# Performance work log

Hardware: AMD Instinct MI355X
Metric: run time of the kernel (lower is better)

Reference implementation:

```python
import jax, jax.numpy as jnp
import numpy as np

NUM_TOKENS = 8192
EMBED_DIM = 32
BETA = 1.0
DECAY = 0.99
L2_EPS = 1e-12  # torch F.normalize denom clamp


def l2norm(t):
    return t / jnp.maximum(jnp.linalg.norm(t, axis=-1, keepdims=True), L2_EPS)


def setup_inputs() -> dict:
    key = jax.random.key(0)
    k1, k2 = jax.random.split(key)
    z = jax.random.normal(k1, (32, EMBED_DIM, 16, 16), dtype=jnp.float32)  # [B, C, H, W]
    embedding = l2norm(jax.random.normal(k2, (NUM_TOKENS, EMBED_DIM), dtype=jnp.float32))
    cluster_sizes = jnp.zeros((NUM_TOKENS,), dtype=jnp.float32)
    return {"z": z, "embedding": embedding, "cluster_sizes": cluster_sizes}


def reference(z, embedding, cluster_sizes):
    B, C, H, W = z.shape
    zc = jnp.transpose(z, (0, 2, 3, 1))          # channel_last: [B, H, W, C]
    zn = l2norm(zc)
    z_flat = zn.reshape(-1, C)                   # [N, C], N = B*H*W

    # nearest centroid by cosine similarity (codebook rows are unit norm)
    cos_sim = z_flat @ embedding.T               # [N, K]
    token_ids = jnp.argmax(cos_sim, axis=-1)     # [N]
    z_q_flat = embedding[token_ids]              # gather, [N, C]
    z_q = z_q_flat.reshape(zn.shape)

    # EMA statistics (training branch; one-hot @ matmuls expressed as scatter-adds)
    bins = jnp.zeros((NUM_TOKENS,), z.dtype).at[token_ids].add(1.0)      # encodings.sum(0)
    new_cluster_sizes = cluster_sizes * DECAY + (1.0 - DECAY) * bins
    zero_mask = bins == 0
    bins_c = jnp.where(zero_mask, 1.0, bins)
    embed_sum = jnp.zeros((NUM_TOKENS, C), z.dtype).at[token_ids].add(z_flat)  # (z_flat.T @ onehot).T
    embed_normalized = l2norm(embed_sum / bins_c[:, None])
    embed_normalized = jnp.where(zero_mask[:, None], embedding, embed_normalized)
    new_embedding = l2norm(embedding * DECAY + (1.0 - DECAY) * embed_normalized)

    # commitment loss + straight-through estimator
    loss = BETA * jnp.mean((jax.lax.stop_gradient(z_q) - zn) ** 2)
    z_q_st = zn + jax.lax.stop_gradient(z_q - zn)
    z_q_out = jnp.transpose(z_q_st, (0, 3, 1, 2))  # back to [B, C, H, W]

    return (z_q_out, loss, token_ids.reshape(B, H, W), new_embedding, new_cluster_sizes)
```

## Files before the change

### kernel.cpp

```cpp
#include <hip/hip_runtime.h>


#define NTOK   8192
#define NCODE  8192
#define CDIM   32
#define HW     256
#define DECAYF 0.99f
#define EPSF   0.01f

#define OUT_ZQ   0
#define OUT_LOSS 262144
#define OUT_IDS  262145
#define OUT_EMB  270337
#define OUT_CS   532481

#define WS_ZN     0u
#define WS_ZNBF   1048576u
#define WS_EBF    1572864u
#define WS_BINS   2097152u
#define WS_LOSSP  2129920u
#define WS_IDS    2130176u
#define WS_POS    2162944u
#define WS_OFFS   2195712u
#define WS_SORTED 2228480u

typedef __attribute__((ext_vector_type(8))) short bf16x8;
typedef __attribute__((ext_vector_type(4))) float f32x4;

__device__ inline unsigned short f2bf(float x) {
    unsigned u = __float_as_uint(x);
    return (unsigned short)((u + 0x7FFFu + ((u >> 16) & 1u)) >> 16);
}
__device__ inline unsigned fmap(float s) {
    unsigned u = __float_as_uint(s);
    return (u & 0x80000000u) ? ~u : (u | 0x80000000u);
}

__global__ __launch_bounds__(256) void k_prep(const float* __restrict__ z,
                                              const float* __restrict__ emb,
                                              float* __restrict__ zn,
                                              unsigned short* __restrict__ znbf,
                                              unsigned short* __restrict__ ebf,
                                              int* __restrict__ bins,
                                              float* __restrict__ loss_part) {
    int bid = blockIdx.x, t = threadIdx.x;
    if (bid < 32) {
        int n = bid * 256 + t;
        int b = n >> 8, hw = n & 255;
        const float* zp = z + (size_t)b * (CDIM * HW) + hw;
        float v[CDIM];
        float ss = 0.f;
#pragma unroll
        for (int c = 0; c < CDIM; ++c) {
            float tv = zp[c * HW];
            v[c] = tv;
            ss += tv * tv;
        }
        float d = fmaxf(sqrtf(ss), 1e-12f);
        float* o = zn + (size_t)n * CDIM;
        unsigned short* ob = znbf + (size_t)n * CDIM;
#pragma unroll
        for (int c = 0; c < CDIM; ++c) {
            float tv = v[c] / d;
            o[c] = tv;
            ob[c] = f2bf(tv);
        }
    } else if (bid < 160) {
        int base = (bid - 32) * 2048 + t * 8;
        const float4* s = (const float4*)(emb + base);
        float4 x4 = s[0], y4 = s[1];
        ushort4 u0 = {f2bf(x4.x), f2bf(x4.y), f2bf(x4.z), f2bf(x4.w)};
        ushort4 u1 = {f2bf(y4.x), f2bf(y4.y), f2bf(y4.z), f2bf(y4.w)};
        *(ushort4*)(ebf + base) = u0;
        *(ushort4*)(ebf + base + 4) = u1;
    } else if (bid < 164) {
        int base = (bid - 160) * 2048 + t;
#pragma unroll
        for (int j = 0; j < 8; ++j) bins[base + j * 256] = 0;
    } else {
        if (t < 64) loss_part[t] = 0.f;
    }
}

__global__ __launch_bounds__(256) void k_argmax(const unsigned short* __restrict__ znbf,
                                                const unsigned short* __restrict__ ebf,
                                                const float* __restrict__ zn,
                                                const float* __restrict__ emb,
                                                int* __restrict__ bins,
                                                int* __restrict__ ids,
                                                int* __restrict__ pos,
                                                float* __restrict__ out,
                                                float* __restrict__ loss_part) {
    __shared__ float gm[4][16];
    __shared__ float thr[16];
    __shared__ unsigned long long bk[16];
    __shared__ int sid[16];
    __shared__ float ls4[4];

    int blk = blockIdx.x, t = threadIdx.x;
    int wave = t >> 6, lane = t & 63;
    int col = lane & 15, quad = lane >> 4;
    int tok0 = blk * 16;

    bf16x8 a = *(const bf16x8*)(znbf + (size_t)(tok0 + col) * CDIM + quad * 8);

    const f32x4 zero4 = {0.f, 0.f, 0.f, 0.f};
    int wbase = wave * 2048;

    float m0 = -1e30f, m1 = -1e30f, m2 = -1e30f, m3 = -1e30f;
#pragma unroll 4
    for (int tt = 0; tt < 128; ++tt) {
        int code = wbase + tt * 16 + col;
        bf16x8 b = *(const bf16x8*)(ebf + (size_t)code * CDIM + quad * 8);
        f32x4 d = __builtin_amdgcn_mfma_f32_16x16x32_bf16(a, b, zero4, 0, 0, 0);
        m0 = fmaxf(m0, d[0]); m1 = fmaxf(m1, d[1]);
        m2 = fmaxf(m2, d[2]); m3 = fmaxf(m3, d[3]);
    }
    {
        float mm[4] = {m0, m1, m2, m3};
#pragma unroll
        for (int r = 0; r < 4; ++r) {
            float v = mm[r];
#pragma unroll
            for (int s = 1; s < 16; s <<= 1) v = fmaxf(v, __shfl_xor(v, s));
            if (col == 0) gm[wave][quad * 4 + r] = v;
        }
    }
    if (t < 16) bk[t] = 0ull;
    __syncthreads();
    if (t < 16)
        thr[t] = fmaxf(fmaxf(gm[0][t], gm[1][t]), fmaxf(gm[2][t], gm[3][t])) - EPSF;
    __syncthreads();

    float th0 = thr[quad * 4 + 0], th1 = thr[quad * 4 + 1];
    float th2 = thr[quad * 4 + 2], th3 = thr[quad * 4 + 3];

#pragma unroll 4
    for (int tt = 0; tt < 128; ++tt) {
        int code = wbase + tt * 16 + col;
        bf16x8 b = *(const bf16x8*)(ebf + (size_t)code * CDIM + quad * 8);
        f32x4 d = __builtin_amdgcn_mfma_f32_16x16x32_bf16(a, b, zero4, 0, 0, 0);
#pragma unroll
        for (int r = 0; r < 4; ++r) {
            float dv = d[r];
            float tv = (r == 0) ? th0 : (r == 1) ? th1 : (r == 2) ? th2 : th3;
            if (dv >= tv) {
                int tl = quad * 4 + r;
                const float* zp = zn + (size_t)(tok0 + tl) * CDIM;
                const float* ep = emb + (size_t)code * CDIM;
                float a0 = 0.f, a1 = 0.f, a2 = 0.f, a3 = 0.f;
#pragma unroll
                for (int j = 0; j < 8; ++j) {
                    a0 = __builtin_fmaf(zp[4 * j + 0], ep[4 * j + 0], a0);
                    a1 = __builtin_fmaf(zp[4 * j + 1], ep[4 * j + 1], a1);
                    a2 = __builtin_fmaf(zp[4 * j + 2], ep[4 * j + 2], a2);
                    a3 = __builtin_fmaf(zp[4 * j + 3], ep[4 * j + 3], a3);
                }
                float s = (a0 + a1) + (a2 + a3);
                unsigned long long key = ((unsigned long long)fmap(s) << 13) |
                                         (unsigned long long)(8191 - code);
                atomicMax(&bk[tl], key);
            }
        }
    }
    __syncthreads();

    if (t < 16) {
        int id = 8191 - (int)(bk[t] & 8191ull);
        sid[t] = id;
        int n = tok0 + t;
        ids[n] = id;
        out[OUT_IDS + n] = (float)id;
        pos[n] = atomicAdd(bins + id, 1);
    }
    __syncthreads();

    float s = 0.f;
#pragma unroll
    for (int i = 0; i < 2; ++i) {
        int tl = i * 8 + (t >> 5);
        int c = t & 31;
        int n = tok0 + tl;
        int id = sid[tl];
        float ev = emb[(size_t)id * CDIM + c];
        float zv = zn[(size_t)n * CDIM + c];
        int b = n >> 8, hw = n & 255;
        out[OUT_ZQ + ((size_t)b * CDIM + c) * HW + hw] = ev;
        float dd = ev - zv;
        s += dd * dd;
    }
#pragma unroll
    for (int off = 32; off > 0; off >>= 1) s += __shfl_down(s, off);
    if (lane == 0) ls4[wave] = s;
    __syncthreads();
    if (t == 0)
        atomicAdd(loss_part + (blk & 63), ls4[0] + ls4[1] + ls4[2] + ls4[3]);
}

__global__ __launch_bounds__(1024) void k_scanplace(const int* __restrict__ bins,
                                                    const int* __restrict__ ids,
                                                    const int* __restrict__ pos,
                                                    int* __restrict__ offs,
                                                    int* __restrict__ sorted) {
    __shared__ int wtot[16], wexcl[16];
    int t = threadIdx.x;
    int lane = t & 63, wid = t >> 6;
    int loc[8];
    int s = 0;
#pragma unroll
    for (int i = 0; i < 8; ++i) {
        loc[i] = s;
        s += bins[t * 8 + i];
    }
    int v = s;
#pragma unroll
    for (int sh = 1; sh < 64; sh <<= 1) {
        int o = __shfl_up(v, sh);
        if (lane >= sh) v += o;
    }
    if (lane == 63) wtot[wid] = v;
    __syncthreads();
    if (t < 16) {
        int w = wtot[t];
        int iv = w;
#pragma unroll
        for (int sh = 1; sh < 16; sh <<= 1) {
            int o = __shfl_up(iv, sh);
            if (t >= sh) iv += o;
        }
        wexcl[t] = iv - w;
    }
    __syncthreads();
    int excl = wexcl[wid] + (v - s);
#pragma unroll
    for (int i = 0; i < 8; ++i) offs[t * 8 + i] = excl + loc[i];
    __syncthreads();
    for (int n = t; n < NTOK; n += 1024)
        sorted[offs[ids[n]] + pos[n]] = n;
}

__global__ __launch_bounds__(256) void k_update(const float* __restrict__ zn,
                                                const float* __restrict__ emb,
                                                const float* __restrict__ cs,
                                                const int* __restrict__ bins,
                                                const int* __restrict__ offs,
                                                const int* __restrict__ sorted,
                                                const float* __restrict__ loss_part,
                                                float* __restrict__ out) {
    int idx = blockIdx.x * 256 + threadIdx.x;
    if (blockIdx.x == 0 && threadIdx.x < 64) {
        float lp = loss_part[threadIdx.x];
#pragma unroll
        for (int sh = 32; sh > 0; sh >>= 1) lp += __shfl_down(lp, sh);
        if (threadIdx.x == 0) out[OUT_LOSS] = lp * (1.0f / 262144.0f);
    }
    int k = idx >> 5, c = idx & 31;
    int bi = bins[k];
    int off = offs[k];
    float t = 0.f;
    for (int i = 0; i < bi; ++i) {
        int n = sorted[off + i];
        t += zn[(size_t)n * CDIM + c];
    }
    float bf = (float)bi;
    bool zero = (bi == 0);
    t /= (zero ? 1.0f : bf);
    float ss = t * t;
#pragma unroll
    for (int s = 1; s < 32; s <<= 1) ss += __shfl_xor(ss, s);
    float d = fmaxf(sqrtf(ss), 1e-12f);
    float ew = emb[idx];
    float en = zero ? ew : (t / d);
    float w = ew * DECAYF + (1.0f - DECAYF) * en;
    float ss2 = w * w;
#pragma unroll
    for (int s = 1; s < 32; s <<= 1) ss2 += __shfl_xor(ss2, s);
    float d2 = fmaxf(sqrtf(ss2), 1e-12f);
    out[OUT_EMB + idx] = w / d2;
    if (c == 0) out[OUT_CS + k] = cs[k] * DECAYF + (1.0f - DECAYF) * bf;
}

extern "C" void kernel_launch(void* const* d_in, const int* in_sizes, int n_in,
                              void* d_out, int out_size, void* d_ws, size_t ws_size,
                              hipStream_t stream) {
    const float* z   = (const float*)d_in[0];
    const float* emb = (const float*)d_in[1];
    const float* cs  = (const float*)d_in[2];
    float* out = (float*)d_out;
    char* ws = (char*)d_ws;

    float* zn            = (float*)(ws + WS_ZN);
    unsigned short* znbf = (unsigned short*)(ws + WS_ZNBF);
    unsigned short* ebf  = (unsigned short*)(ws + WS_EBF);
    int* bins            = (int*)(ws + WS_BINS);
    float* loss_part     = (float*)(ws + WS_LOSSP);
    int* ids             = (int*)(ws + WS_IDS);
    int* pos             = (int*)(ws + WS_POS);
    int* offs            = (int*)(ws + WS_OFFS);
    int* sorted          = (int*)(ws + WS_SORTED);

    k_prep<<<dim3(165), 256, 0, stream>>>(z, emb, zn, znbf, ebf, bins, loss_part);
    k_argmax<<<dim3(NTOK / 16), 256, 0, stream>>>(znbf, ebf, zn, emb, bins, ids,
                                                  pos, out, loss_part);
    k_scanplace<<<dim3(1), 1024, 0, stream>>>(bins, ids, pos, offs, sorted);
    k_update<<<dim3(1024), 256, 0, stream>>>(zn, emb, cs, bins, offs, sorted,
                                             loss_part, out);
}
```

Before: 142.9 us.

## Stage codebook in double-buffered LDS and process 32 tokens per block

The argmax kernel now copies 256-code bf16 chunks of the codebook into a double-buffered shared-memory tile and reuses each B fragment across two 16-token MFMA tiles. Each block handles 32 tokens instead of 16, which halves the number of times the codebook is streamed from global memory across the grid. The cost is 32 KB of LDS per block, a barrier per chunk, and half as many blocks (256), which may reduce occupancy and latency hiding on a device with 256 CUs.

```diff
diff --git a/kernel.cpp b/kernel.cpp
--- a/kernel.cpp
+++ b/kernel.cpp
@@ -23,6 +23,9 @@
 #define WS_POS    2162944u
 #define WS_OFFS   2195712u
 #define WS_SORTED 2228480u
+
+#define CHUNK  256
+#define NCHUNK (NCODE / CHUNK)
 
 typedef __attribute__((ext_vector_type(8))) short bf16x8;
 typedef __attribute__((ext_vector_type(4))) float f32x4;
@@ -91,81 +94,132 @@
                                                 int* __restrict__ pos,
                                                 float* __restrict__ out,
                                                 float* __restrict__ loss_part) {
-    __shared__ float gm[4][16];
-    __shared__ float thr[16];
-    __shared__ unsigned long long bk[16];
-    __shared__ int sid[16];
+    __shared__ unsigned short lbs[2][CHUNK * CDIM];
+    __shared__ float gm[4][32];
+    __shared__ float thr[32];
+    __shared__ unsigned long long bk[32];
+    __shared__ int sid[32];
     __shared__ float ls4[4];
 
     int blk = blockIdx.x, t = threadIdx.x;
     int wave = t >> 6, lane = t & 63;
     int col = lane & 15, quad = lane >> 4;
-    int tok0 = blk * 16;
-
-    bf16x8 a = *(const bf16x8*)(znbf + (size_t)(tok0 + col) * CDIM + quad * 8);
+    int tok0 = blk * 32;
+
+    bf16x8 a[2];
+#pragma unroll
+    for (int f = 0; f < 2; ++f)
+        a[f] = *(const bf16x8*)(znbf + (size_t)(tok0 + f * 16 + col) * CDIM + quad * 8);
 
     const f32x4 zero4 = {0.f, 0.f, 0.f, 0.f};
-    int wbase = wave * 2048;
-
-    float m0 = -1e30f, m1 = -1e30f, m2 = -1e30f, m3 = -1e30f;
-#pragma unroll 4
-    for (int tt = 0; tt < 128; ++tt) {
-        int code = wbase + tt * 16 + col;
-        bf16x8 b = *(const bf16x8*)(ebf + (size_t)code * CDIM + quad * 8);
-        f32x4 d = __builtin_amdgcn_mfma_f32_16x16x32_bf16(a, b, zero4, 0, 0, 0);
-        m0 = fmaxf(m0, d[0]); m1 = fmaxf(m1, d[1]);
-        m2 = fmaxf(m2, d[2]); m3 = fmaxf(m3, d[3]);
-    }
+    const float4* esrc = (const float4*)ebf;
+
     {
-        float mm[4] = {m0, m1, m2, m3};
+        float4* dst = (float4*)lbs[0];
+#pragma unroll
+        for (int j = 0; j < 4; ++j) dst[t + j * 256] = esrc[t + j * 256];
+    }
+    __syncthreads();
+
+    float m[2][4];
+#pragma unroll
+    for (int f = 0; f < 2; ++f)
+#pragma unroll
+        for (int r = 0; r < 4; ++r) m[f][r] = -1e30f;
+
+    for (int ch = 0; ch < NCHUNK; ++ch) {
+        int buf = ch & 1;
+        if (ch + 1 < NCHUNK) {
+            float4* dst = (float4*)lbs[buf ^ 1];
+            const float4* src = esrc + (size_t)(ch + 1) * 1024;
+#pragma unroll
+            for (int j = 0; j < 4; ++j) dst[t + j * 256] = src[t + j * 256];
+        }
+        const bf16x8* bl = (const bf16x8*)lbs[buf];
+#pragma unroll
+        for (int i = 0; i < 4; ++i) {
+            int tile = wave + i * 4;
+            bf16x8 b = bl[(tile * 16 + col) * 4 + quad];
+#pragma unroll
+            for (int f = 0; f < 2; ++f) {
+                f32x4 d = __builtin_amdgcn_mfma_f32_16x16x32_bf16(a[f], b, zero4, 0, 0, 0);
+#pragma unroll
+                for (int r = 0; r < 4; ++r) m[f][r] = fmaxf(m[f][r], d[r]);
+            }
+        }
+        __syncthreads();
+    }
+#pragma unroll
+    for (int f = 0; f < 2; ++f)
 #pragma unroll
         for (int r = 0; r < 4; ++r) {
-            float v = mm[r];
+            float v = m[f][r];
 #pragma unroll
             for (int s = 1; s < 16; s <<= 1) v = fmaxf(v, __shfl_xor(v, s));
-            if (col == 0) gm[wave][quad * 4 + r] = v;
-        }
-    }
-    if (t < 16) bk[t] = 0ull;
-    __syncthreads();
-    if (t < 16)
+            if (col == 0) gm[wave][f * 16 + quad * 4 + r] = v;
+        }
+    if (t < 32) bk[t] = 0ull;
+    __syncthreads();
+    if (t < 32)
         thr[t] = fmaxf(fmaxf(gm[0][t], gm[1][t]), fmaxf(gm[2][t], gm[3][t])) - EPSF;
     __syncthreads();
 
-    float th0 = thr[quad * 4 + 0], th1 = thr[quad * 4 + 1];
-    float th2 = thr[quad * 4 + 2], th3 = thr[quad * 4 + 3];
-
-#pragma unroll 4
-    for (int tt = 0; tt < 128; ++tt) {
-        int code = wbase + tt * 16 + col;
-        bf16x8 b = *(const bf16x8*)(ebf + (size_t)code * CDIM + quad * 8);
-        f32x4 d = __builtin_amdgcn_mfma_f32_16x16x32_bf16(a, b, zero4, 0, 0, 0);
-#pragma unroll
-        for (int r = 0; r < 4; ++r) {
-            float dv = d[r];
-            float tv = (r == 0) ? th0 : (r == 1) ? th1 : (r == 2) ? th2 : th3;
-            if (dv >= tv) {
-                int tl = quad * 4 + r;
-                const float* zp = zn + (size_t)(tok0 + tl) * CDIM;
-                const float* ep = emb + (size_t)code * CDIM;
-                float a0 = 0.f, a1 = 0.f, a2 = 0.f, a3 = 0.f;
-#pragma unroll
-                for (int j = 0; j < 8; ++j) {
-                    a0 = __builtin_fmaf(zp[4 * j + 0], ep[4 * j + 0], a0);
-                    a1 = __builtin_fmaf(zp[4 * j + 1], ep[4 * j + 1], a1);
-                    a2 = __builtin_fmaf(zp[4 * j + 2], ep[4 * j + 2], a2);
-                    a3 = __builtin_fmaf(zp[4 * j + 3], ep[4 * j + 3], a3);
+    float th[2][4];
+#pragma unroll
+    for (int f = 0; f < 2; ++f)
+#pragma unroll
+        for (int r = 0; r < 4; ++r) th[f][r] = thr[f * 16 + quad * 4 + r];
+
+    {
+        float4* dst = (float4*)lbs[0];
+#pragma unroll
+        for (int j = 0; j < 4; ++j) dst[t + j * 256] = esrc[t + j * 256];
+    }
+    __syncthreads();
+    for (int ch = 0; ch < NCHUNK; ++ch) {
+        int buf = ch & 1;
+        if (ch + 1 < NCHUNK) {
+            float4* dst = (float4*)lbs[buf ^ 1];
+            const float4* src = esrc + (size_t)(ch + 1) * 1024;
+#pragma unroll
+            for (int j = 0; j < 4; ++j) dst[t + j * 256] = src[t + j * 256];
+        }
+        const bf16x8* bl = (const bf16x8*)lbs[buf];
+#pragma unroll
+        for (int i = 0; i < 4; ++i) {
+            int tile = wave + i * 4;
+            bf16x8 b = bl[(tile * 16 + col) * 4 + quad];
+#pragma unroll
+            for (int f = 0; f < 2; ++f) {
+                f32x4 d = __builtin_amdgcn_mfma_f32_16x16x32_bf16(a[f], b, zero4, 0, 0, 0);
+#pragma unroll
+                for (int r = 0; r < 4; ++r) {
+                    if (d[r] >= th[f][r]) {
+                        int tl = f * 16 + quad * 4 + r;
+                        int code = ch * CHUNK + tile * 16 + col;
+                        const float* zp = zn + (size_t)(tok0 + tl) * CDIM;
+                        const float* ep = emb + (size_t)code * CDIM;
+                        float a0 = 0.f, a1 = 0.f, a2 = 0.f, a3 = 0.f;
+#pragma unroll
+                        for (int j = 0; j < 8; ++j) {
+                            a0 = __builtin_fmaf(zp[4 * j + 0], ep[4 * j + 0], a0);
+                            a1 = __builtin_fmaf(zp[4 * j + 1], ep[4 * j + 1], a1);
+                            a2 = __builtin_fmaf(zp[4 * j + 2], ep[4 * j + 2], a2);
+                            a3 = __builtin_fmaf(zp[4 * j + 3], ep[4 * j + 3], a3);
+                        }
+                        float s = (a0 + a1) + (a2 + a3);
+                        unsigned long long key =
+                            ((unsigned long long)fmap(s) << 13) |
+                            (unsigned long long)(8191 - code);
+                        atomicMax(&bk[tl], key);
+                    }
                 }
-                float s = (a0 + a1) + (a2 + a3);
-                unsigned long long key = ((unsigned long long)fmap(s) << 13) |
-                                         (unsigned long long)(8191 - code);
-                atomicMax(&bk[tl], key);
             }
         }
-    }
-    __syncthreads();
-
-    if (t < 16) {
+        __syncthreads();
+    }
+
+    if (t < 32) {
         int id = 8191 - (int)(bk[t] & 8191ull);
         sid[t] = id;
         int n = tok0 + t;
@@ -177,7 +231,7 @@
 
     float s = 0.f;
 #pragma unroll
-    for (int i = 0; i < 2; ++i) {
+    for (int i = 0; i < 4; ++i) {
         int tl = i * 8 + (t >> 5);
         int c = t & 31;
         int n = tok0 + tl;
@@ -300,7 +354,7 @@
     int* sorted          = (int*)(ws + WS_SORTED);
 
     k_prep<<<dim3(165), 256, 0, stream>>>(z, emb, zn, znbf, ebf, bins, loss_part);
-    k_argmax<<<dim3(NTOK / 16), 256, 0, stream>>>(znbf, ebf, zn, emb, bins, ids,
+    k_argmax<<<dim3(NTOK / 32), 256, 0, stream>>>(znbf, ebf, zn, emb, bins, ids,
                                                   pos, out, loss_part);
     k_scanplace<<<dim3(1), 1024, 0, stream>>>(bins, ids, pos, offs, sorted);
     k_update<<<dim3(1024), 256, 0, stream>>>(zn, emb, cs, bins, offs, sorted,
```

After: 168.1 us. 17.6% more time.
